# Kernel tuning notes

Measured on AMD Instinct MI355X. Metric: run time of the kernel, lower is better.

The kernel has to match this reference:

```python
import jax, jax.numpy as jnp
import numpy as np

K = 20  # hard-coded in DGCNN.__init__

def _pd_neg(x):
    # negative squared pairwise distance, [B,N,C] -> [B,N,N]
    inner = jnp.einsum('bnc,bmc->bnm', x, x)
    sq = jnp.sum(x * x, axis=-1)
    return 2.0 * inner - sq[:, :, None] - sq[:, None, :]

def _knn(x):
    return jax.lax.top_k(_pd_neg(x), K)[1]  # [B,N,K]

def _edge_feat(x, idx):
    # x: [B,N,C], idx: [B,N,K] -> [B,N,K,2C] = concat(central, neighbor-central)
    nb = jax.vmap(lambda p, i: p[i])(x, idx)
    c = x[:, :, None, :]
    return jnp.concatenate([jnp.broadcast_to(c, nb.shape), nb - c], axis=-1)

def _conv(x, w, b, act=True):
    # 1x1 Conv2d == per-point linear; BN at inference with init stats is identity
    y = jnp.einsum('...c,cd->...d', x, w) + b
    return jax.nn.relu(y) if act else y

def _forward(x, tw1, tb1, tw2, tb2, tw3, tb3, tfw1, tfb1, tfw2, tfb2, txw, txb,
             e1w1, e1b1, e1w2, e1b2, e2w1, e2b1, e2w2, e2b2, e3w1, e3b1,
             c1w, c1b, c2w, c2b, c3w, c3b, c4w, c4b):
    pts = x[:, :, :3]
    # spatial transform net on edge features of raw xyz
    ef = _edge_feat(pts, _knn(pts))                      # [B,N,K,6]
    t = _conv(_conv(ef, tw1, tb1), tw2, tb2)
    t = jnp.max(t, axis=2)                               # max over neighbors
    t = _conv(t, tw3, tb3)                               # [B,N,1024]
    t = jnp.max(t, axis=1)                               # global maxpool -> [B,1024]
    t = jax.nn.relu(t @ tfw1 + tfb1)
    t = jax.nn.relu(t @ tfw2 + tfb2)
    xf = (t @ txw + txb).reshape(-1, 3, 3)
    p = jnp.einsum('bnc,bcd->bnd', pts, xf)              # transformed points
    # EdgeConv 1
    ef = _edge_feat(p, _knn(p))                          # [B,N,K,6]
    x1 = jnp.max(_conv(_conv(ef, e1w1, e1b1), e1w2, e1b2), axis=2)   # [B,N,64]
    # EdgeConv 2
    ef = _edge_feat(x1, _knn(x1))                        # [B,N,K,128]
    x2 = jnp.max(_conv(_conv(ef, e2w1, e2b1), e2w2, e2b2), axis=2)
    # EdgeConv 3
    ef = _edge_feat(x2, _knn(x2))
    x3 = jnp.max(_conv(ef, e3w1, e3b1), axis=2)
    # global feature + per-point head
    net = _conv(jnp.concatenate([x1, x2, x3], axis=-1), c1w, c1b)    # [B,N,1024]
    g = jnp.max(net, axis=1, keepdims=True)              # maxpool over all points
    g = jnp.broadcast_to(g, (g.shape[0], x1.shape[1], g.shape[2]))
    net = jnp.concatenate([g, x1, x2, x3], axis=-1)      # [B,N,1216]
    net = _conv(net, c2w, c2b)
    net = _conv(net, c3w, c3b)
    # dropout is identity at inference (training=False)
    return _conv(net, c4w, c4b, act=False)               # [B,N,num_classes]

def setup_inputs():
    keys = iter(jax.random.split(jax.random.key(0), 64))
    def w(*shape):
        return jax.random.normal(next(keys), shape, jnp.float32) / np.float32(np.sqrt(shape[0]))
    def b(n):
        return 0.01 * jax.random.normal(next(keys), (n,), jnp.float32)
    B, N, F = 4, 4096, 6
    d = dict(x=jax.random.normal(next(keys), (B, N, F), jnp.float32))
    d.update(tw1=w(6, 64), tb1=b(64), tw2=w(64, 128), tb2=b(128), tw3=w(128, 1024), tb3=b(1024),
             tfw1=w(1024, 512), tfb1=b(512), tfw2=w(512, 256), tfb2=b(256),
             txw=0.01 * w(256, 9), txb=jnp.eye(3, dtype=jnp.float32).reshape(9))
    d.update(e1w1=w(6, 64), e1b1=b(64), e1w2=w(64, 64), e1b2=b(64),
             e2w1=w(128, 64), e2b1=b(64), e2w2=w(64, 64), e2b2=b(64),
             e3w1=w(128, 64), e3b1=b(64))
    d.update(c1w=w(192, 1024), c1b=b(1024), c2w=w(1216, 512), c2b=b(512),
             c3w=w(512, 256), c3b=b(256), c4w=w(256, 2), c4b=b(2))
    return d

def reference(x, tw1, tb1, tw2, tb2, tw3, tb3, tfw1, tfb1, tfw2, tfb2, txw, txb,
              e1w1, e1b1, e1w2, e1b2, e2w1, e2b1, e2w2, e2b2, e3w1, e3b1,
              c1w, c1b, c2w, c2b, c3w, c3b, c4w, c4b):
    return _forward(x, tw1, tb1, tw2, tb2, tw3, tb3, tfw1, tfb1, tfw2, tfb2, txw, txb,
                    e1w1, e1b1, e1w2, e1b2, e2w1, e2b1, e2w2, e2b2, e3w1, e3b1,
                    c1w, c1b, c2w, c2b, c3w, c3b, c4w, c4b)
```

## Files before the change

kernel.cpp:

```cpp
#include <hip/hip_runtime.h>

#define Nn 4096
#define KK 20
#define BN 16384

typedef __attribute__((ext_vector_type(8))) short bf16x8;
typedef __attribute__((ext_vector_type(4))) float f32x4;

__device__ __forceinline__ unsigned short f2bf(float f) {
  unsigned int x = __float_as_uint(f);
  return (unsigned short)((x + 0x7fffu + ((x >> 16) & 1u)) >> 16);
}
__device__ __forceinline__ float bf2f(unsigned short u) {
  return __uint_as_float(((unsigned int)u) << 16);
}

#define INS5(dd, tt)                                                         \
  if (dd > m5) {                                                             \
    if (dd > m3) {                                                           \
      if (dd > m1) { m5=m4;t5=t4; m4=m3;t4=t3; m3=m2;t3=t2; m2=m1;t2=t1; m1=dd;t1=tt; } \
      else if (dd > m2) { m5=m4;t5=t4; m4=m3;t4=t3; m3=m2;t3=t2; m2=dd;t2=tt; } \
      else { m5=m4;t5=t4; m4=m3;t4=t3; m3=dd;t3=tt; }                        \
    } else if (dd > m4) { m5=m4;t5=t4; m4=dd;t4=tt; }                        \
    else { m5=dd; t5=tt; }                                                   \
  }

__device__ __forceinline__ void cvtT_j(const float* __restrict__ src,
                                       unsigned short* __restrict__ dst,
                                       int N, int K, int ldn, int row0, int i) {
  if (i >= N * K) return;
  int n = i / K, k = i - n * K;
  dst[i] = f2bf(src[(size_t)(row0 + k) * ldn + n]);
}
__device__ __forceinline__ void cvtT3_j(const float* __restrict__ src,
                                        unsigned short* __restrict__ h,
                                        unsigned short* __restrict__ m,
                                        unsigned short* __restrict__ l,
                                        int N, int K, int ldn, int i) {
  if (i >= N * K) return;
  int n = i / K, k = i - n * K;
  float x = src[(size_t)k * ldn + n];
  unsigned short hh = f2bf(x); float xh = bf2f(hh);
  unsigned short mm = f2bf(x - xh); float xm = bf2f(mm);
  unsigned short ll = f2bf(x - xh - xm);
  h[i] = hh; m[i] = mm; l[i] = ll;
}
__device__ __forceinline__ void prepD_j(const float* __restrict__ w1,
                                        float* __restrict__ Md, int i) {
  if (i >= 8192) return;
  int j = i >> 7, c = i & 127;
  Md[i] = (c < 64) ? (w1[j * 64 + c] - w1[(64 + j) * 64 + c]) : w1[(64 + j) * 64 + (c - 64)];
}

__global__ __launch_bounds__(256) void k_prepAll(
    const float* __restrict__ xin, float* __restrict__ pts,
    const float* __restrict__ W22, unsigned short* __restrict__ c1wT,
    const float* __restrict__ W24, unsigned short* __restrict__ c2wT,
    const float* __restrict__ W26, unsigned short* __restrict__ c3wT,
    const float* __restrict__ W4, unsigned short* __restrict__ w3Th,
    unsigned short* __restrict__ w3Tm, unsigned short* __restrict__ w3Tl,
    const float* __restrict__ W2, unsigned short* __restrict__ tw2h,
    unsigned short* __restrict__ tw2m, unsigned short* __restrict__ tw2l,
    const float* __restrict__ W14, unsigned short* __restrict__ e1h,
    unsigned short* __restrict__ e1m, unsigned short* __restrict__ e1l,
    const float* __restrict__ W18, unsigned short* __restrict__ e2h,
    unsigned short* __restrict__ e2m, unsigned short* __restrict__ e2l,
    const float* __restrict__ W6, unsigned short* __restrict__ fw1h,
    unsigned short* __restrict__ fw1m, unsigned short* __restrict__ fw1l,
    unsigned short* __restrict__ cw2h, unsigned short* __restrict__ cw2m,
    unsigned short* __restrict__ cw2l,
    const float* __restrict__ W8, unsigned short* __restrict__ fw2h,
    unsigned short* __restrict__ fw2m, unsigned short* __restrict__ fw2l,
    const float* __restrict__ W16, float* __restrict__ MdC,
    const float* __restrict__ W20, float* __restrict__ MdD) {
  int blk = blockIdx.x, t = threadIdx.x;
  if (blk < 768) { cvtT_j(W22, c1wT, 1024, 192, 1024, 0, blk * 256 + t); return; }
  blk -= 768;
  if (blk < 384) { cvtT_j(W24, c2wT, 512, 192, 512, 1024, blk * 256 + t); return; }
  blk -= 384;
  if (blk < 512) { cvtT_j(W26, c3wT, 256, 512, 256, 0, blk * 256 + t); return; }
  blk -= 512;
  if (blk < 512) { cvtT3_j(W4, w3Th, w3Tm, w3Tl, 1024, 128, 1024, blk * 256 + t); return; }
  blk -= 512;
  if (blk < 32) { cvtT3_j(W2, tw2h, tw2m, tw2l, 128, 64, 128, blk * 256 + t); return; }
  blk -= 32;
  if (blk < 16) { cvtT3_j(W14, e1h, e1m, e1l, 64, 64, 64, blk * 256 + t); return; }
  blk -= 16;
  if (blk < 16) { cvtT3_j(W18, e2h, e2m, e2l, 64, 64, 64, blk * 256 + t); return; }
  blk -= 16;
  if (blk < 2048) { cvtT3_j(W6, fw1h, fw1m, fw1l, 512, 1024, 512, blk * 256 + t); return; }
  blk -= 2048;
  if (blk < 2048) { cvtT3_j(W24, cw2h, cw2m, cw2l, 512, 1024, 512, blk * 256 + t); return; }
  blk -= 2048;
  if (blk < 512) { cvtT3_j(W8, fw2h, fw2m, fw2l, 256, 512, 256, blk * 256 + t); return; }
  blk -= 512;
  if (blk < 32) { prepD_j(W16, MdC, blk * 256 + t); return; }
  blk -= 32;
  if (blk < 32) { prepD_j(W20, MdD, blk * 256 + t); return; }
  blk -= 32;
  {
    int i = blk * 256 + t;
    if (i < BN * 3) {
      int pt = i / 3, c = i - 3 * pt;
      pts[i] = xin[pt * 6 + c];
    }
  }
}

__global__ void k_tv3(const float* __restrict__ part, const float* __restrict__ bias,
                      unsigned short* __restrict__ h, unsigned short* __restrict__ m,
                      unsigned short* __restrict__ l) {
  int i = blockIdx.x * 256 + threadIdx.x;
  if (i >= 16 * 1024) return;
  int row = i >> 10, col = i & 1023;
  float v = 0.f;
  if (row < 4) {
    float mx = -INFINITY;
#pragma unroll 8
    for (int s = 0; s < 32; ++s) mx = fmaxf(mx, part[((size_t)row * 32 + s) * 1024 + col]);
    v = fmaxf(mx + bias[col], 0.f);
  }
  unsigned short hh = f2bf(v); float xh = bf2f(hh);
  unsigned short mm = f2bf(v - xh); float xm = bf2f(mm);
  unsigned short ll = f2bf(v - xh - xm);
  h[i] = hh; m[i] = mm; l[i] = ll;
}

__global__ void k_pad3(const float* __restrict__ src, int rows, int cols,
                       unsigned short* __restrict__ h, unsigned short* __restrict__ m,
                       unsigned short* __restrict__ l) {
  int i = blockIdx.x * 256 + threadIdx.x;
  if (i >= 16 * cols) return;
  int row = i / cols, col = i - row * cols;
  float v = (row < rows) ? src[(size_t)row * cols + col] : 0.f;
  unsigned short hh = f2bf(v); float xh = bf2f(hh);
  unsigned short mm = f2bf(v - xh); float xm = bf2f(mm);
  unsigned short ll = f2bf(v - xh - xm);
  h[i] = hh; m[i] = mm; l[i] = ll;
}

template <int N, int K, int SEG>
__global__ __launch_bounds__(256) void k_gemmSK(const unsigned short* __restrict__ Ah,
                                                const unsigned short* __restrict__ Am,
                                                const unsigned short* __restrict__ Al,
                                                const unsigned short* __restrict__ Bh,
                                                const unsigned short* __restrict__ Bm,
                                                const unsigned short* __restrict__ Bl,
                                                float* __restrict__ partial) {
  constexpr int KSEG = K / SEG;
  constexpr int KS = KSEG / 32;
  int t = threadIdx.x;
  int wv = t >> 6, lane = t & 63;
  int quad = lane >> 4, l16 = lane & 15;
  int bx = blockIdx.x;
  int nb = bx / SEG, seg = bx - nb * SEG;
  int col = nb * 64 + wv * 16 + l16;
  int k0 = seg * KSEG;
  size_t wo = (size_t)col * K + k0 + quad * 8;
  size_t ao = (size_t)l16 * K + k0 + quad * 8;
  f32x4 acc = {0.f, 0.f, 0.f, 0.f};
#pragma unroll
  for (int s = 0; s < KS; ++s) {
    bf16x8 xh = *(const bf16x8*)(Ah + ao + s * 32);
    bf16x8 xm = *(const bf16x8*)(Am + ao + s * 32);
    bf16x8 xl = *(const bf16x8*)(Al + ao + s * 32);
    bf16x8 wh = *(const bf16x8*)(Bh + wo + s * 32);
    bf16x8 wm = *(const bf16x8*)(Bm + wo + s * 32);
    bf16x8 wl = *(const bf16x8*)(Bl + wo + s * 32);
    acc = __builtin_amdgcn_mfma_f32_16x16x32_bf16(xh, wh, acc, 0, 0, 0);
    acc = __builtin_amdgcn_mfma_f32_16x16x32_bf16(xh, wm, acc, 0, 0, 0);
    acc = __builtin_amdgcn_mfma_f32_16x16x32_bf16(xm, wh, acc, 0, 0, 0);
    acc = __builtin_amdgcn_mfma_f32_16x16x32_bf16(xh, wl, acc, 0, 0, 0);
    acc = __builtin_amdgcn_mfma_f32_16x16x32_bf16(xl, wh, acc, 0, 0, 0);
    acc = __builtin_amdgcn_mfma_f32_16x16x32_bf16(xm, wm, acc, 0, 0, 0);
  }
  if (quad == 0) {
#pragma unroll
    for (int r = 0; r < 4; ++r)
      partial[((size_t)seg * 4 + r) * N + col] = acc[r];
  }
}

__global__ void k_redS(const float* __restrict__ partial, const float* __restrict__ bias,
                       float* __restrict__ outp, int N, int SEG, int relu) {
  int i = blockIdx.x * 256 + threadIdx.x;
  if (i >= 4 * N) return;
  int r = i / N, c = i - r * N;
  float s = 0.f;
  for (int seg = 0; seg < SEG; ++seg) s += partial[((size_t)seg * 4 + r) * N + c];
  if (bias) s += bias[c];
  if (relu) s = fmaxf(s, 0.f);
  outp[(size_t)r * N + c] = s;
}

__global__ __launch_bounds__(256) void k_fc3p(const float* __restrict__ h2, const float* __restrict__ txw,
                                              const float* __restrict__ txb, const float* __restrict__ pts,
                                              float* __restrict__ p) {
  __shared__ float sh2[256];
  __shared__ float sxf[9];
  int t = threadIdx.x;
  int b = blockIdx.x;
  sh2[t] = h2[(size_t)b * 256 + t];
  __syncthreads();
  if (t < 9) {
    float acc = txb[t];
    for (int j = 0; j < 256; ++j) acc = fmaf(sh2[j], txw[j * 9 + t], acc);
    sxf[t] = acc;
  }
  __syncthreads();
  for (int n = t; n < Nn; n += 256) {
    const float* pr = pts + ((size_t)b * Nn + n) * 3;
    float a0 = pr[0], a1 = pr[1], a2 = pr[2];
    float* po = p + ((size_t)b * Nn + n) * 3;
#pragma unroll
    for (int d = 0; d < 3; ++d) po[d] = a0 * sxf[d] + a1 * sxf[3 + d] + a2 * sxf[6 + d];
  }
}

__device__ __forceinline__ float dist4(const float4* __restrict__ tile4, int c,
                                       float qx, float qy, float qz, float qsq) {
  float4 v = tile4[c];
  float dot = fmaf(qx, v.x, fmaf(qy, v.y, qz * v.z));
  return 2.0f * dot - qsq - v.w;
}

__global__ __launch_bounds__(1024) void k_knn3(const float* __restrict__ src, int* __restrict__ idx) {
  __shared__ float4 tile4[Nn];
  int t = threadIdx.x;
  int wave = t >> 6, lane = t & 63;
  int g = blockIdx.x * 16 + wave;
  int b = g >> 12, n = g & (Nn - 1);
  const float* base = src + (size_t)b * Nn * 3;
  for (int e = t; e < Nn; e += 1024) {
    float x = base[e * 3], y = base[e * 3 + 1], z = base[e * 3 + 2];
    tile4[e] = make_float4(x, y, z, fmaf(x, x, fmaf(y, y, z * z)));
  }
  __syncthreads();
  float4 q4 = tile4[n];
  float qx = q4.x, qy = q4.y, qz = q4.z, qsq = q4.w;
  float m1 = -INFINITY, m2 = -INFINITY, m3 = -INFINITY, m4 = -INFINITY, m5 = -INFINITY;
  int t1 = 0, t2 = 0, t3 = 0, t4 = 0, t5 = 0;
#pragma unroll 4
  for (int tt = 0; tt < 64; ++tt) {
    float dd = dist4(tile4, (tt << 6) + lane, qx, qy, qz, qsq);
    INS5(dd, tt)
  }
  unsigned long long removed = 0ull;
  int cnt = 5;
  int sel = 0;
#pragma unroll 1
  for (int k = 0; k < 20; ++k) {
    float v = m1; int ci = (t1 << 6) | lane;
    float mx = v;
#pragma unroll
    for (int off = 32; off; off >>= 1) mx = fmaxf(mx, __shfl_xor(mx, off, 64));
    int cand = (v == mx) ? ci : 0x7FFFFFFF;
#pragma unroll
    for (int off = 32; off; off >>= 1) cand = min(cand, __shfl_xor(cand, off, 64));
    if (k == lane) sel = cand;
    if (cand == ci) {
      removed |= 1ull << t1;
      if (cnt > 1) { m1 = m2; t1 = t2; m2 = m3; t2 = t3; m3 = m4; t3 = t4; m4 = m5; t4 = t5; --cnt; }
      else {
        m1 = -INFINITY; m2 = -INFINITY; m3 = -INFINITY; m4 = -INFINITY; m5 = -INFINITY;
        t1 = 0; t2 = 0; t3 = 0; t4 = 0; t5 = 0;
#pragma unroll 1
        for (int tt = 0; tt < 64; ++tt) {
          if ((removed >> tt) & 1ull) continue;
          float dd = dist4(tile4, (tt << 6) + lane, qx, qy, qz, qsq);
          INS5(dd, tt)
        }
        cnt = 5;
      }
    }
  }
  if (lane < 20) idx[(size_t)g * KK + lane] = sel;
}

__global__ void k_sqnorm(const float* __restrict__ src, float* __restrict__ out) {
  int g = blockIdx.x * 256 + threadIdx.x;
  if (g >= BN) return;
  const float4* r = (const float4*)(src + (size_t)g * 64);
  float s = 0.f;
#pragma unroll
  for (int j = 0; j < 16; ++j) { float4 v = r[j]; s += v.x * v.x + v.y * v.y + v.z * v.z + v.w * v.w; }
  out[g] = s;
}

__device__ __forceinline__ void topk_d5(const float (&d)[64],
                                        float m1, int t1, float m2, int t2, float m3, int t3,
                                        float m4, int t4, float m5, int t5,
                                        int lane, int* __restrict__ op) {
  unsigned long long removed = 0ull;
  int cnt = 5;
  int sel = 0;
#pragma unroll 1
  for (int k = 0; k < 20; ++k) {
    float v = m1; int ci = (t1 << 6) | lane;
    float mx = v;
#pragma unroll
    for (int off = 32; off; off >>= 1) mx = fmaxf(mx, __shfl_xor(mx, off, 64));
    int cand = (v == mx) ? ci : 0x7FFFFFFF;
#pragma unroll
    for (int off = 32; off; off >>= 1) cand = min(cand, __shfl_xor(cand, off, 64));
    if (k == lane) sel = cand;
    if (cand == ci) {
      removed |= 1ull << t1;
      if (cnt > 1) { m1 = m2; t1 = t2; m2 = m3; t2 = t3; m3 = m4; t3 = t4; m4 = m5; t4 = t5; --cnt; }
      else {
        m1 = -INFINITY; m2 = -INFINITY; m3 = -INFINITY; m4 = -INFINITY; m5 = -INFINITY;
        t1 = 0; t2 = 0; t3 = 0; t4 = 0; t5 = 0;
#pragma unroll
        for (int tt = 0; tt < 64; ++tt) {
          if (!((removed >> tt) & 1ull)) {
            float dd = d[tt];
            INS5(dd, tt)
          }
        }
        cnt = 5;
      }
    }
  }
  if (lane < 20) op[lane] = sel;
}

__global__ __launch_bounds__(1024) void k_dsel(const unsigned short* __restrict__ Xh,
                                               const unsigned short* __restrict__ Xm,
                                               const unsigned short* __restrict__ Xl,
                                               const float* __restrict__ sq,
                                               int* __restrict__ idx) {
  __shared__ float sD[16 * 1284];
  int t = threadIdx.x;
  int wave = t >> 6, lane = t & 63;
  int quad = lane >> 4, l16 = lane & 15;
  int blk = blockIdx.x;
  int b = blk >> 8, rs = blk & 255;
  int r0 = rs * 16;
  const size_t base = (size_t)b * Nn * 64;
  const float* sqb = sq + b * Nn;
  bf16x8 ah[2], am[2], al[2];
#pragma unroll
  for (int ks = 0; ks < 2; ++ks) {
    size_t ra = base + (size_t)(r0 + l16) * 64 + ks * 32 + quad * 8;
    ah[ks] = *(const bf16x8*)(Xh + ra);
    am[ks] = *(const bf16x8*)(Xm + ra);
    al[ks] = *(const bf16x8*)(Xl + ra);
  }
  float sqr[4];
#pragma unroll
  for (int r = 0; r < 4; ++r) sqr[r] = sqb[r0 + quad * 4 + r];
  float d[64];
  float m1 = -INFINITY, m2 = -INFINITY, m3 = -INFINITY, m4 = -INFINITY, m5 = -INFINITY;
  int t1 = 0, t2 = 0, t3 = 0, t4 = 0, t5 = 0;
#pragma unroll
  for (int ch = 0; ch < 4; ++ch) {
#pragma unroll
    for (int tt = 0; tt < 4; ++tt) {
      int cc = wave * 64 + tt * 16;
      int cb = ch * 1024 + cc;
      f32x4 acc = {0.f, 0.f, 0.f, 0.f};
#pragma unroll
      for (int ks = 0; ks < 2; ++ks) {
        size_t rb = base + (size_t)(cb + l16) * 64 + ks * 32 + quad * 8;
        bf16x8 bh = *(const bf16x8*)(Xh + rb);
        bf16x8 bm = *(const bf16x8*)(Xm + rb);
        bf16x8 bl = *(const bf16x8*)(Xl + rb);
        acc = __builtin_amdgcn_mfma_f32_16x16x32_bf16(ah[ks], bh, acc, 0, 0, 0);
        acc = __builtin_amdgcn_mfma_f32_16x16x32_bf16(ah[ks], bm, acc, 0, 0, 0);
        acc = __builtin_amdgcn_mfma_f32_16x16x32_bf16(am[ks], bh, acc, 0, 0, 0);
        acc = __builtin_amdgcn_mfma_f32_16x16x32_bf16(ah[ks], bl, acc, 0, 0, 0);
        acc = __builtin_amdgcn_mfma_f32_16x16x32_bf16(al[ks], bh, acc, 0, 0, 0);
        acc = __builtin_amdgcn_mfma_f32_16x16x32_bf16(am[ks], bm, acc, 0, 0, 0);
      }
      float sqc = sqb[cb + l16];
#pragma unroll
      for (int r = 0; r < 4; ++r)
        sD[(quad * 4 + r) * 1284 + cc + l16] = 2.0f * acc[r] - sqr[r] - sqc;
    }
    __syncthreads();
#pragma unroll
    for (int jj = 0; jj < 16; ++jj) {
      int tt = ch * 16 + jj;
      float dd = sD[wave * 1284 + jj * 64 + lane];
      d[tt] = dd;
      INS5(dd, tt)
    }
    __syncthreads();
  }
  topk_d5(d, m1, t1, m2, t2, m3, t3, m4, t4, m5, t5, lane,
          idx + (size_t)(b * Nn + r0 + wave) * KK);
}

__global__ __launch_bounds__(256) void k_uv3(const float* __restrict__ pts, const float* __restrict__ w1,
                                             const float* __restrict__ b1, float* __restrict__ uvb) {
  __shared__ float sw[384];
  __shared__ float sb[64];
  int t = threadIdx.x;
  for (int e = t; e < 384; e += 256) sw[e] = w1[e];
  if (t < 64) sb[t] = b1[t];
  __syncthreads();
  int pl = t >> 6, c = t & 63;
  int p = blockIdx.x * 4 + pl;
  const float* pr = pts + (size_t)p * 3;
  float x0 = pr[0], x1 = pr[1], x2 = pr[2];
  float wb0 = sw[192 + c], wb1 = sw[256 + c], wb2 = sw[320 + c];
  float v = x0 * wb0 + x1 * wb1 + x2 * wb2;
  float u = sb[c] + x0 * (sw[c] - wb0) + x1 * (sw[64 + c] - wb1) + x2 * (sw[128 + c] - wb2);
  uvb[(size_t)p * 128 + c] = u;
  uvb[(size_t)p * 128 + 64 + c] = v;
}

__global__ __launch_bounds__(256) void k_uv(const float* __restrict__ x2, const float* __restrict__ Md,
                                            const float* __restrict__ bias, float* __restrict__ uv) {
  __shared__ float sM[8192];
  __shared__ float sx[32 * 68];
  int t = threadIdx.x;
  for (int e = t; e < 8192; e += 256) sM[e] = Md[e];
  int p0 = blockIdx.x * 32;
  for (int e = t; e < 512; e += 256) {
    int r = e >> 4, c4 = e & 15;
    *(float4*)(sx + r * 68 + c4 * 4) = *(const float4*)(x2 + (size_t)(p0 + r) * 64 + c4 * 4);
  }
  __syncthreads();
  int c = t & 127, rg = t >> 7;
  float badd = (c < 64) ? bias[c] : 0.f;
  float accv[16];
#pragma unroll
  for (int r = 0; r < 16; ++r) accv[r] = 0.f;
#pragma unroll
  for (int jc = 0; jc < 8; ++jc) {
    float mreg[8];
#pragma unroll
    for (int q = 0; q < 8; ++q) mreg[q] = sM[(jc * 8 + q) * 128 + c];
#pragma unroll
    for (int r = 0; r < 16; ++r) {
      const float* xr = sx + (rg * 16 + r) * 68 + jc * 8;
      float4 a = *(const float4*)xr, bb = *(const float4*)(xr + 4);
      float s = accv[r];
      s = fmaf(a.x, mreg[0], s); s = fmaf(a.y, mreg[1], s);
      s = fmaf(a.z, mreg[2], s); s = fmaf(a.w, mreg[3], s);
      s = fmaf(bb.x, mreg[4], s); s = fmaf(bb.y, mreg[5], s);
      s = fmaf(bb.z, mreg[6], s); s = fmaf(bb.w, mreg[7], s);
      accv[r] = s;
    }
  }
#pragma unroll
  for (int r = 0; r < 16; ++r)
    uv[(size_t)(p0 + rg * 16 + r) * 128 + c] = accv[r] + badd;
}

template <int NOUT, bool WRITEF, bool SPLIT3, bool CAT>
__global__ __launch_bounds__(256, 4) void k_econv(const float* __restrict__ uv,
                                                  const int* __restrict__ idx,
                                                  const unsigned short* __restrict__ W2h,
                                                  const unsigned short* __restrict__ W2m,
                                                  const unsigned short* __restrict__ W2l,
                                                  const float* __restrict__ b2,
                                                  float* __restrict__ outF,
                                                  unsigned short* __restrict__ oh,
                                                  unsigned short* __restrict__ om,
                                                  unsigned short* __restrict__ ol,
                                                  unsigned short* __restrict__ ocat,
                                                  int catoff) {
  __shared__ unsigned short y3[4][3][20 * 72];
  int t = threadIdx.x;
  int wv = t >> 6, lane = t & 63;
  int quad = lane >> 4, l16 = lane & 15;
  int p0 = blockIdx.x * 4;
  int p = p0 + wv;
  size_t nbase = (size_t)(p >> 12) * Nn;
  constexpr int CT = NOUT / 64;
  bf16x8 wfh[CT][2], wfm[CT][2], wfl[CT][2];
#pragma unroll
  for (int ct = 0; ct < CT; ++ct)
#pragma unroll
    for (int ks = 0; ks < 2; ++ks) {
      size_t wo = (size_t)(wv * (CT * 16) + ct * 16 + l16) * 64 + ks * 32 + quad * 8;
      wfh[ct][ks] = *(const bf16x8*)(W2h + wo);
      wfm[ct][ks] = *(const bf16x8*)(W2m + wo);
      wfl[ct][ks] = *(const bf16x8*)(W2l + wo);
    }
  const int* ip = idx + (size_t)p * KK;
  float u = uv[(size_t)p * 128 + lane];
  unsigned short* yh = y3[wv][0];
  unsigned short* ym = y3[wv][1];
  unsigned short* yl = y3[wv][2];
  float vv[20];
#pragma unroll
  for (int k = 0; k < 20; ++k) {
    int nb = ip[k];
    vv[k] = uv[(nbase + nb) * 128 + 64 + lane];
  }
#pragma unroll
  for (int k = 0; k < 20; ++k) {
    float y = fmaxf(u + vv[k], 0.f);
    unsigned short hh = f2bf(y); float fh = bf2f(hh);
    unsigned short mm = f2bf(y - fh); float fm = bf2f(mm);
    unsigned short ll = f2bf(y - fh - fm);
    yh[k * 72 + lane] = hh;
    ym[k * 72 + lane] = mm;
    yl[k * 72 + lane] = ll;
  }
  __syncthreads();
#pragma unroll 1
  for (int pp = 0; pp < 4; ++pp) {
    const unsigned short* ph0 = y3[pp][0];
    const unsigned short* pm0 = y3[pp][1];
    const unsigned short* pl0 = y3[pp][2];
    f32x4 acc[CT][2];
#pragma unroll
    for (int ct = 0; ct < CT; ++ct) {
      acc[ct][0] = (f32x4){0.f, 0.f, 0.f, 0.f};
      acc[ct][1] = (f32x4){0.f, 0.f, 0.f, 0.f};
    }
#pragma unroll
    for (int ks = 0; ks < 2; ++ks) {
      bf16x8 ah[2], am[2], al[2];
#pragma unroll
      for (int mt = 0; mt < 2; ++mt) {
        int row = mt * 16 + l16;
        int rr = (row < 20) ? row : 0;
        int aoff = rr * 72 + ks * 32 + quad * 8;
        ah[mt] = *(const bf16x8*)(ph0 + aoff);
        am[mt] = *(const bf16x8*)(pm0 + aoff);
        al[mt] = *(const bf16x8*)(pl0 + aoff);
      }
#pragma unroll
      for (int ct = 0; ct < CT; ++ct)
#pragma unroll
        for (int mt = 0; mt < 2; ++mt) {
          f32x4 a = acc[ct][mt];
          a = __builtin_amdgcn_mfma_f32_16x16x32_bf16(ah[mt], wfh[ct][ks], a, 0, 0, 0);
          a = __builtin_amdgcn_mfma_f32_16x16x32_bf16(ah[mt], wfm[ct][ks], a, 0, 0, 0);
          a = __builtin_amdgcn_mfma_f32_16x16x32_bf16(am[mt], wfh[ct][ks], a, 0, 0, 0);
          a = __builtin_amdgcn_mfma_f32_16x16x32_bf16(ah[mt], wfl[ct][ks], a, 0, 0, 0);
          a = __builtin_amdgcn_mfma_f32_16x16x32_bf16(al[mt], wfh[ct][ks], a, 0, 0, 0);
          a = __builtin_amdgcn_mfma_f32_16x16x32_bf16(am[mt], wfm[ct][ks], a, 0, 0, 0);
          acc[ct][mt] = a;
        }
    }
    int pt = p0 + pp;
#pragma unroll
    for (int ct = 0; ct < CT; ++ct) {
      int col = wv * (CT * 16) + ct * 16 + l16;
      float m0 = fmaxf(fmaxf(acc[ct][0][0], acc[ct][0][1]), fmaxf(acc[ct][0][2], acc[ct][0][3]));
      float m1v = (quad == 0)
                      ? fmaxf(fmaxf(acc[ct][1][0], acc[ct][1][1]), fmaxf(acc[ct][1][2], acc[ct][1][3]))
                      : -INFINITY;
      float m = fmaxf(m0, m1v);
      m = fmaxf(m, __shfl_xor(m, 16, 64));
      m = fmaxf(m, __shfl_xor(m, 32, 64));
      if (quad == 0) {
        float v = fmaxf(m + b2[col], 0.f);
        if (WRITEF) outF[(size_t)pt * NOUT + col] = v;
        if (SPLIT3) {
          unsigned short hh = f2bf(v); float fh = bf2f(hh);
          unsigned short mm2 = f2bf(v - fh); float fm = bf2f(mm2);
          unsigned short ll = f2bf(v - fh - fm);
          oh[(size_t)pt * NOUT + col] = hh;
          om[(size_t)pt * NOUT + col] = mm2;
          ol[(size_t)pt * NOUT + col] = ll;
        }
        if (CAT) ocat[(size_t)pt * 192 + catoff + col] = f2bf(v);
      }
    }
  }
}

__global__ __launch_bounds__(256) void k_gmax(const float* __restrict__ uv, const int* __restrict__ idx,
                                              unsigned short* __restrict__ ocat) {
  __shared__ int sidx[4][20];
  int t = threadIdx.x;
  int pl = t >> 6, c = t & 63;
  int p0 = blockIdx.x * 4;
  if (t < 80) sidx[t / 20][t % 20] = idx[(size_t)(p0 + t / 20) * KK + (t % 20)];
  __syncthreads();
  int p = p0 + pl;
  size_t nbase = (size_t)(p >> 12) * Nn;
  float u = uv[(size_t)p * 128 + c];
  float m = -INFINITY;
#pragma unroll
  for (int k = 0; k < 20; ++k) m = fmaxf(m, uv[(nbase + sidx[pl][k]) * 128 + 64 + c]);
  ocat[(size_t)p * 192 + 128 + c] = f2bf(fmaxf(u + m, 0.f));
}

template <int K>
__global__ __launch_bounds__(256) void k_mgemm(const unsigned short* __restrict__ A,
                                               const unsigned short* __restrict__ WT,
                                               float* __restrict__ outp) {
  constexpr int KS = K / 32;
  int t = threadIdx.x;
  int wv = t >> 6, lane = t & 63;
  int quad = lane >> 4, l16 = lane & 15;
  int blk = blockIdx.x;
  int b = blk >> 9, cb = (blk >> 5) & 15, ns = blk & 31;
  int n0 = cb * 64 + wv * 16;
  bf16x8 bfr[KS];
  const unsigned short* wrow = WT + (size_t)(n0 + l16) * K + quad * 8;
#pragma unroll
  for (int s = 0; s < KS; ++s) bfr[s] = *(const bf16x8*)(wrow + s * 32);
  const unsigned short* Ab = A + ((size_t)b * Nn + ns * 128 + l16) * K + quad * 8;
  float rmax = -INFINITY;
#pragma unroll 2
  for (int mt = 0; mt < 8; ++mt) {
    const unsigned short* ar = Ab + (size_t)mt * 16 * K;
    f32x4 acc = {0.f, 0.f, 0.f, 0.f};
#pragma unroll
    for (int s = 0; s < KS; ++s) {
      bf16x8 af = *(const bf16x8*)(ar + s * 32);
      acc = __builtin_amdgcn_mfma_f32_16x16x32_bf16(af, bfr[s], acc, 0, 0, 0);
    }
    rmax = fmaxf(rmax, fmaxf(fmaxf(acc[0], acc[1]), fmaxf(acc[2], acc[3])));
  }
  rmax = fmaxf(rmax, __shfl_xor(rmax, 16, 64));
  rmax = fmaxf(rmax, __shfl_xor(rmax, 32, 64));
  if (quad == 0) outp[((size_t)b * 32 + ns) * 1024 + n0 + l16] = rmax;
}

template <int K>
__global__ __launch_bounds__(256) void k_mgemm3s(const unsigned short* __restrict__ Ah,
                                                 const unsigned short* __restrict__ Am,
                                                 const unsigned short* __restrict__ Al,
                                                 const unsigned short* __restrict__ Bh,
                                                 const unsigned short* __restrict__ Bm,
                                                 const unsigned short* __restrict__ Bl,
                                                 float* __restrict__ outp) {
  constexpr int KS = K / 32;
  int t = threadIdx.x;
  int wv = t >> 6, lane = t & 63;
  int quad = lane >> 4, l16 = lane & 15;
  int blk = blockIdx.x;
  int b = blk >> 9, cb = (blk >> 5) & 15, ns = blk & 31;
  int n0 = cb * 64 + wv * 16;
  bf16x8 wh[KS], wm[KS], wl[KS];
  size_t wo = (size_t)(n0 + l16) * K + quad * 8;
#pragma unroll
  for (int s = 0; s < KS; ++s) {
    wh[s] = *(const bf16x8*)(Bh + wo + s * 32);
    wm[s] = *(const bf16x8*)(Bm + wo + s * 32);
    wl[s] = *(const bf16x8*)(Bl + wo + s * 32);
  }
  size_t ao = ((size_t)b * Nn + ns * 128 + l16) * K + quad * 8;
  float rmax = -INFINITY;
#pragma unroll 1
  for (int mt = 0; mt < 8; ++mt) {
    size_t ar = ao + (size_t)mt * 16 * K;
    f32x4 acc = {0.f, 0.f, 0.f, 0.f};
#pragma unroll
    for (int s = 0; s < KS; ++s) {
      bf16x8 xh = *(const bf16x8*)(Ah + ar + s * 32);
      bf16x8 xm = *(const bf16x8*)(Am + ar + s * 32);
      bf16x8 xl = *(const bf16x8*)(Al + ar + s * 32);
      acc = __builtin_amdgcn_mfma_f32_16x16x32_bf16(xh, wh[s], acc, 0, 0, 0);
      acc = __builtin_amdgcn_mfma_f32_16x16x32_bf16(xh, wm[s], acc, 0, 0, 0);
      acc = __builtin_amdgcn_mfma_f32_16x16x32_bf16(xm, wh[s], acc, 0, 0, 0);
      acc = __builtin_amdgcn_mfma_f32_16x16x32_bf16(xh, wl[s], acc, 0, 0, 0);
      acc = __builtin_amdgcn_mfma_f32_16x16x32_bf16(xl, wh[s], acc, 0, 0, 0);
      acc = __builtin_amdgcn_mfma_f32_16x16x32_bf16(xm, wm[s], acc, 0, 0, 0);
    }
    rmax = fmaxf(rmax, fmaxf(fmaxf(acc[0], acc[1]), fmaxf(acc[2], acc[3])));
  }
  rmax = fmaxf(rmax, __shfl_xor(rmax, 16, 64));
  rmax = fmaxf(rmax, __shfl_xor(rmax, 32, 64));
  if (quad == 0) outp[((size_t)b * 32 + ns) * 1024 + n0 + l16] = rmax;
}

__global__ __launch_bounds__(256) void k_final(const unsigned short* __restrict__ xcat,
                                               const float* __restrict__ gc,
                                               const float* __restrict__ c2b,
                                               const unsigned short* __restrict__ c2wT,
                                               const unsigned short* __restrict__ c3wT,
                                               const float* __restrict__ c3b,
                                               const float* __restrict__ c4w, const float* __restrict__ c4b,
                                               float* __restrict__ out) {
  __shared__ unsigned short z5[16 * 520];
  __shared__ float z2[16 * 260];
  int t = threadIdx.x;
  int wv = t >> 6, lane = t & 63;
  int quad = lane >> 4, l16 = lane & 15;
  int p0 = blockIdx.x * 16;
  int b = p0 >> 12;
  bf16x8 a1[6];
  const unsigned short* ar = xcat + (size_t)(p0 + l16) * 192 + quad * 8;
#pragma unroll
  for (int s = 0; s < 6; ++s) a1[s] = *(const bf16x8*)(ar + s * 32);
#pragma unroll 1
  for (int ntw = 0; ntw < 8; ++ntw) {
    int col = wv * 128 + ntw * 16 + l16;
    float bias = gc[(size_t)b * 512 + col] + c2b[col];
    f32x4 acc = {bias, bias, bias, bias};
    const unsigned short* wr = c2wT + (size_t)col * 192 + quad * 8;
#pragma unroll
    for (int s = 0; s < 6; ++s) {
      bf16x8 bfr = *(const bf16x8*)(wr + s * 32);
      acc = __builtin_amdgcn_mfma_f32_16x16x32_bf16(a1[s], bfr, acc, 0, 0, 0);
    }
#pragma unroll
    for (int r = 0; r < 4; ++r)
      z5[(quad * 4 + r) * 520 + col] = f2bf(fmaxf(acc[r], 0.f));
  }
  __syncthreads();
  bf16x8 a2[16];
#pragma unroll
  for (int s = 0; s < 16; ++s) a2[s] = *(const bf16x8*)(z5 + l16 * 520 + s * 32 + quad * 8);
#pragma unroll 1
  for (int ntw = 0; ntw < 4; ++ntw) {
    int col = wv * 64 + ntw * 16 + l16;
    float bias = c3b[col];
    f32x4 acc = {bias, bias, bias, bias};
    const unsigned short* wr = c3wT + (size_t)col * 512 + quad * 8;
#pragma unroll
    for (int s = 0; s < 16; ++s) {
      bf16x8 bfr = *(const bf16x8*)(wr + s * 32);
      acc = __builtin_amdgcn_mfma_f32_16x16x32_bf16(a2[s], bfr, acc, 0, 0, 0);
    }
#pragma unroll
    for (int r = 0; r < 4; ++r)
      z2[(quad * 4 + r) * 260 + col] = fmaxf(acc[r], 0.f);
  }
  __syncthreads();
  if (t < 32) {
    int m = t >> 1, e = t & 1;
    float acc = c4b[e];
    const float* zr = z2 + m * 260;
    for (int j = 0; j < 256; ++j) acc = fmaf(zr[j], c4w[j * 2 + e], acc);
    out[(size_t)(p0 + m) * 2 + e] = acc;
  }
}

extern "C" void kernel_launch(void* const* d_in, const int* in_sizes, int n_in,
                              void* d_out, int out_size, void* d_ws, size_t ws_size,
                              hipStream_t stream) {
  const float* xin = (const float*)d_in[0];
  const float* W[30];
  for (int i = 0; i < 30; ++i) W[i] = (const float*)d_in[i + 1];

  float* ws = (float*)d_ws;
  size_t off = 0;
  float* pts   = ws + off; off += (size_t)BN * 3;
  float* p     = ws + off; off += (size_t)BN * 3;
  int*   idx   = (int*)(ws + off); off += (size_t)BN * KK;
  float* sq    = ws + off; off += BN;
  float* dpart = ws + off; off += 4 * 32 * 1024;
  float* h1    = ws + off; off += 4 * 512;
  float* h2b   = ws + off; off += 4 * 256;
  float* x1    = ws + off; off += (size_t)BN * 64;
  float* x2    = ws + off; off += (size_t)BN * 64;
  float* gpart = ws + off; off += 4 * 32 * 1024;
  float* gc    = ws + off; off += 4 * 512;
  float* uvb   = ws + off; off += (size_t)BN * 128;
  float* partial = ws + off; off += 16 * 4 * 512;
  unsigned short* xcat = (unsigned short*)(ws + off); off += (size_t)BN * 96;
  unsigned short* c1wT = (unsigned short*)(ws + off); off += 98304;
  unsigned short* c2wT = (unsigned short*)(ws + off); off += 49152;
  unsigned short* c3wT = (unsigned short*)(ws + off); off += 65536;
  unsigned short* w3Th = (unsigned short*)(ws + off); off += 65536;
  unsigned short* w3Tm = (unsigned short*)(ws + off); off += 65536;
  unsigned short* w3Tl = (unsigned short*)(ws + off); off += 65536;
  unsigned short* tw2h = (unsigned short*)(ws + off); off += 4096;
  unsigned short* tw2m = (unsigned short*)(ws + off); off += 4096;
  unsigned short* tw2l = (unsigned short*)(ws + off); off += 4096;
  unsigned short* e1h  = (unsigned short*)(ws + off); off += 2048;
  unsigned short* e1m  = (unsigned short*)(ws + off); off += 2048;
  unsigned short* e1l  = (unsigned short*)(ws + off); off += 2048;
  unsigned short* e2h  = (unsigned short*)(ws + off); off += 2048;
  unsigned short* e2m  = (unsigned short*)(ws + off); off += 2048;
  unsigned short* e2l  = (unsigned short*)(ws + off); off += 2048;
  unsigned short* xsh  = (unsigned short*)(ws + off); off += 524288;
  unsigned short* xsm  = (unsigned short*)(ws + off); off += 524288;
  unsigned short* xsl  = (unsigned short*)(ws + off); off += 524288;
  float* MdC   = ws + off; off += 8192;
  float* MdD   = ws + off; off += 8192;
  unsigned short* fw1h = (unsigned short*)(ws + off); off += 262144;
  unsigned short* fw1m = (unsigned short*)(ws + off); off += 262144;
  unsigned short* fw1l = (unsigned short*)(ws + off); off += 262144;
  unsigned short* cw2h = (unsigned short*)(ws + off); off += 262144;
  unsigned short* cw2m = (unsigned short*)(ws + off); off += 262144;
  unsigned short* cw2l = (unsigned short*)(ws + off); off += 262144;
  unsigned short* fw2h = (unsigned short*)(ws + off); off += 65536;
  unsigned short* fw2m = (unsigned short*)(ws + off); off += 65536;
  unsigned short* fw2l = (unsigned short*)(ws + off); off += 65536;
  unsigned short* tvh  = (unsigned short*)(ws + off); off += 8192;
  unsigned short* tvm  = (unsigned short*)(ws + off); off += 8192;
  unsigned short* tvl  = (unsigned short*)(ws + off); off += 8192;
  unsigned short* h13h = (unsigned short*)(ws + off); off += 4096;
  unsigned short* h13m = (unsigned short*)(ws + off); off += 4096;
  unsigned short* h13l = (unsigned short*)(ws + off); off += 4096;
  float* Dbuf  = ws + off; off += (size_t)Nn * Nn;
  unsigned short* t3h = (unsigned short*)Dbuf;
  unsigned short* t3m = t3h + (size_t)BN * 128;
  unsigned short* t3l = t3m + (size_t)BN * 128;

  k_prepAll<<<dim3(7104), dim3(256), 0, stream>>>(
      xin, pts,
      W[22], c1wT, W[24], c2wT, W[26], c3wT,
      W[4], w3Th, w3Tm, w3Tl,
      W[2], tw2h, tw2m, tw2l,
      W[14], e1h, e1m, e1l,
      W[18], e2h, e2m, e2l,
      W[6], fw1h, fw1m, fw1l,
      cw2h, cw2m, cw2l,
      W[8], fw2h, fw2m, fw2l,
      W[16], MdC, W[20], MdD);

  k_knn3<<<dim3(1024), dim3(1024), 0, stream>>>(pts, idx);
  k_uv3<<<dim3(4096), dim3(256), 0, stream>>>(pts, W[0], W[1], uvb);
  k_econv<128, false, true, false><<<dim3(4096), dim3(256), 0, stream>>>(
      uvb, idx, tw2h, tw2m, tw2l, W[3], nullptr, t3h, t3m, t3l, nullptr, 0);
  k_mgemm3s<128><<<dim3(2048), dim3(256), 0, stream>>>(t3h, t3m, t3l, w3Th, w3Tm, w3Tl, dpart);
  k_tv3<<<dim3(64), dim3(256), 0, stream>>>(dpart, W[5], tvh, tvm, tvl);
  k_gemmSK<512, 1024, 16><<<dim3(128), dim3(256), 0, stream>>>(tvh, tvm, tvl, fw1h, fw1m, fw1l, partial);
  k_redS<<<dim3(8), dim3(256), 0, stream>>>(partial, W[7], h1, 512, 16, 1);
  k_pad3<<<dim3(32), dim3(256), 0, stream>>>(h1, 4, 512, h13h, h13m, h13l);
  k_gemmSK<256, 512, 8><<<dim3(32), dim3(256), 0, stream>>>(h13h, h13m, h13l, fw2h, fw2m, fw2l, partial);
  k_redS<<<dim3(4), dim3(256), 0, stream>>>(partial, W[9], h2b, 256, 8, 1);
  k_fc3p<<<dim3(4), dim3(256), 0, stream>>>(h2b, W[10], W[11], pts, p);

  k_knn3<<<dim3(1024), dim3(1024), 0, stream>>>(p, idx);
  k_uv3<<<dim3(4096), dim3(256), 0, stream>>>(p, W[12], W[13], uvb);
  k_econv<64, true, true, true><<<dim3(4096), dim3(256), 0, stream>>>(
      uvb, idx, e1h, e1m, e1l, W[15], x1, xsh, xsm, xsl, xcat, 0);
  k_sqnorm<<<dim3(64), dim3(256), 0, stream>>>(x1, sq);
  k_dsel<<<dim3(1024), dim3(1024), 0, stream>>>(xsh, xsm, xsl, sq, idx);
  k_uv<<<dim3(512), dim3(256), 0, stream>>>(x1, MdC, W[17], uvb);
  k_econv<64, true, true, true><<<dim3(4096), dim3(256), 0, stream>>>(
      uvb, idx, e2h, e2m, e2l, W[19], x2, xsh, xsm, xsl, xcat, 64);
  k_sqnorm<<<dim3(64), dim3(256), 0, stream>>>(x2, sq);
  k_dsel<<<dim3(1024), dim3(1024), 0, stream>>>(xsh, xsm, xsl, sq, idx);
  k_uv<<<dim3(512), dim3(256), 0, stream>>>(x2, MdD, W[21], uvb);
  k_gmax<<<dim3(4096), dim3(256), 0, stream>>>(uvb, idx, xcat);

  k_mgemm<192><<<dim3(2048), dim3(256), 0, stream>>>(xcat, c1wT, gpart);
  k_tv3<<<dim3(64), dim3(256), 0, stream>>>(gpart, W[23], tvh, tvm, tvl);
  k_gemmSK<512, 1024, 16><<<dim3(128), dim3(256), 0, stream>>>(tvh, tvm, tvl, cw2h, cw2m, cw2l, partial);
  k_redS<<<dim3(8), dim3(256), 0, stream>>>(partial, nullptr, gc, 512, 16, 0);
  k_final<<<dim3(1024), dim3(256), 0, stream>>>(xcat, gc, W[25], c2wT, c3wT,
                                                W[27], W[28], W[29], (float*)d_out);
}
```

Measured before the change: 1.234 ms.

## Replace block-wide kNN select with per-wave streaming top-6 plus fallback fix kernel

The 64-dim kNN selection now gives each wave 16 query rows and streams all 4096 candidates through MFMA tiles. Each lane keeps a register top-6 per row over its column slice, with no shared-memory distance matrix and no block barriers. The 20 nearest are picked by a 16-lane shuffle merge. If a lane's 6 slots run out before 20 are chosen, the row is flagged and recomputed exactly by a separate k_dfix kernel, which costs an extra launch of 2048 mostly-empty blocks and a memset, and relies on rows being flagged only rarely.

```diff
diff --git a/kernel.cpp b/kernel.cpp
--- a/kernel.cpp
+++ b/kernel.cpp
@@ -3,6 +3,7 @@
 #define Nn 4096
 #define KK 20
 #define BN 16384
+#define FCAP 2048
 
 typedef __attribute__((ext_vector_type(8))) short bf16x8;
 typedef __attribute__((ext_vector_type(4))) float f32x4;
@@ -23,6 +24,50 @@
       else { m5=m4;t5=t4; m4=m3;t4=t3; m3=dd;t3=tt; }                        \
     } else if (dd > m4) { m5=m4;t5=t4; m4=dd;t4=tt; }                        \
     else { m5=dd; t5=tt; }                                                   \
+  }
+
+#define INS6(M1,C1,M2,C2,M3,C3,M4,C4,M5,C5,M6,C6, dd, cc)                    \
+  if (dd > M6) {                                                             \
+    if (dd > M3) {                                                           \
+      if (dd > M1) { M6=M5;C6=C5; M5=M4;C5=C4; M4=M3;C4=C3; M3=M2;C3=C2; M2=M1;C2=C1; M1=dd;C1=cc; } \
+      else if (dd > M2) { M6=M5;C6=C5; M5=M4;C5=C4; M4=M3;C4=C3; M3=M2;C3=C2; M2=dd;C2=cc; } \
+      else { M6=M5;C6=C5; M5=M4;C5=C4; M4=M3;C4=C3; M3=dd;C3=cc; }           \
+    } else if (dd > M5) {                                                    \
+      if (dd > M4) { M6=M5;C6=C5; M5=M4;C5=C4; M4=dd;C4=cc; }                \
+      else { M6=M5;C6=C5; M5=dd;C5=cc; }                                     \
+    } else { M6=dd; C6=cc; }                                                 \
+  }
+
+#define POPREG(M1,C1,M2,C2,M3,C3,M4,C4,M5,C5,M6,C6, RR)                      \
+  {                                                                          \
+    int cnt = 6; int selA = 0, selB = 0; bool fail = false;                  \
+    for (int k = 0; k < 20; ++k) {                                           \
+      float v = M1; int ci = C1;                                             \
+      float mx = v;                                                          \
+      mx = fmaxf(mx, __shfl_xor(mx, 1, 64));                                 \
+      mx = fmaxf(mx, __shfl_xor(mx, 2, 64));                                 \
+      mx = fmaxf(mx, __shfl_xor(mx, 4, 64));                                 \
+      mx = fmaxf(mx, __shfl_xor(mx, 8, 64));                                 \
+      int cand = (v == mx) ? ci : 0x7FFFFFFF;                                \
+      cand = min(cand, __shfl_xor(cand, 1, 64));                             \
+      cand = min(cand, __shfl_xor(cand, 2, 64));                             \
+      cand = min(cand, __shfl_xor(cand, 4, 64));                             \
+      cand = min(cand, __shfl_xor(cand, 8, 64));                             \
+      if (l16 == k) selA = cand;                                             \
+      if (k >= 16 && l16 == (k - 16)) selB = cand;                           \
+      if (v == mx && ci == cand) {                                           \
+        if (cnt > 1) { M1=M2;C1=C2; M2=M3;C2=C3; M3=M4;C3=C4; M4=M5;C4=C5; M5=M6;C5=C6; M6=-INFINITY; --cnt; } \
+        else { M1 = -INFINITY; if (k < 19) fail = true; }                    \
+      }                                                                      \
+    }                                                                        \
+    int rowg = r0 + quad * 4 + RR;                                           \
+    idx[(size_t)rowg * KK + l16] = selA;                                     \
+    if (l16 < 4) idx[(size_t)rowg * KK + 16 + l16] = selB;                   \
+    unsigned long long fm = __ballot(fail);                                  \
+    if (l16 == 0) {                                                          \
+      unsigned grp = (unsigned)((fm >> (quad * 16)) & 0xFFFFull);            \
+      if (grp) { int pf = atomicAdd(flagc, 1); if (pf < FCAP) flagr[pf] = rowg; } \
+    }                                                                        \
   }
 
 __device__ __forceinline__ void cvtT_j(const float* __restrict__ src,
@@ -287,10 +332,130 @@
   out[g] = s;
 }
 
-__device__ __forceinline__ void topk_d5(const float (&d)[64],
-                                        float m1, int t1, float m2, int t2, float m3, int t3,
-                                        float m4, int t4, float m5, int t5,
-                                        int lane, int* __restrict__ op) {
+__global__ __launch_bounds__(256) void k_dselW(const unsigned short* __restrict__ Xh,
+                                               const unsigned short* __restrict__ Xm,
+                                               const unsigned short* __restrict__ Xl,
+                                               const float* __restrict__ sq,
+                                               int* __restrict__ flagc,
+                                               int* __restrict__ flagr,
+                                               int* __restrict__ idx) {
+  int t = threadIdx.x;
+  int wv = t >> 6, lane = t & 63;
+  int quad = lane >> 4, l16 = lane & 15;
+  int gw = blockIdx.x * 4 + wv;
+  int r0 = gw * 16;
+  int b = r0 >> 12;
+  int n0 = r0 & (Nn - 1);
+  const size_t base = (size_t)b * Nn * 64;
+  const float* sqb = sq + (size_t)b * Nn;
+  bf16x8 ah[2], am[2], al[2];
+#pragma unroll
+  for (int ks = 0; ks < 2; ++ks) {
+    size_t ra = base + (size_t)(n0 + l16) * 64 + ks * 32 + quad * 8;
+    ah[ks] = *(const bf16x8*)(Xh + ra);
+    am[ks] = *(const bf16x8*)(Xm + ra);
+    al[ks] = *(const bf16x8*)(Xl + ra);
+  }
+  float sqr0 = sqb[n0 + quad * 4 + 0];
+  float sqr1 = sqb[n0 + quad * 4 + 1];
+  float sqr2 = sqb[n0 + quad * 4 + 2];
+  float sqr3 = sqb[n0 + quad * 4 + 3];
+  float aM1=-INFINITY,aM2=-INFINITY,aM3=-INFINITY,aM4=-INFINITY,aM5=-INFINITY,aM6=-INFINITY;
+  float bM1=-INFINITY,bM2=-INFINITY,bM3=-INFINITY,bM4=-INFINITY,bM5=-INFINITY,bM6=-INFINITY;
+  float cM1=-INFINITY,cM2=-INFINITY,cM3=-INFINITY,cM4=-INFINITY,cM5=-INFINITY,cM6=-INFINITY;
+  float dM1=-INFINITY,dM2=-INFINITY,dM3=-INFINITY,dM4=-INFINITY,dM5=-INFINITY,dM6=-INFINITY;
+  int aC1=0,aC2=0,aC3=0,aC4=0,aC5=0,aC6=0;
+  int bC1=0,bC2=0,bC3=0,bC4=0,bC5=0,bC6=0;
+  int cC1=0,cC2=0,cC3=0,cC4=0,cC5=0,cC6=0;
+  int dC1=0,dC2=0,dC3=0,dC4=0,dC5=0,dC6=0;
+#pragma unroll 2
+  for (int tile = 0; tile < 256; ++tile) {
+    int cb = tile * 16;
+    f32x4 acc = {0.f, 0.f, 0.f, 0.f};
+#pragma unroll
+    for (int ks = 0; ks < 2; ++ks) {
+      size_t rb = base + (size_t)(cb + l16) * 64 + ks * 32 + quad * 8;
+      bf16x8 bh = *(const bf16x8*)(Xh + rb);
+      bf16x8 bm = *(const bf16x8*)(Xm + rb);
+      bf16x8 bl = *(const bf16x8*)(Xl + rb);
+      acc = __builtin_amdgcn_mfma_f32_16x16x32_bf16(ah[ks], bh, acc, 0, 0, 0);
+      acc = __builtin_amdgcn_mfma_f32_16x16x32_bf16(ah[ks], bm, acc, 0, 0, 0);
+      acc = __builtin_amdgcn_mfma_f32_16x16x32_bf16(am[ks], bh, acc, 0, 0, 0);
+      acc = __builtin_amdgcn_mfma_f32_16x16x32_bf16(ah[ks], bl, acc, 0, 0, 0);
+      acc = __builtin_amdgcn_mfma_f32_16x16x32_bf16(al[ks], bh, acc, 0, 0, 0);
+      acc = __builtin_amdgcn_mfma_f32_16x16x32_bf16(am[ks], bm, acc, 0, 0, 0);
+    }
+    float sqc = sqb[cb + l16];
+    int cc = cb + l16;
+    float dd0 = 2.0f * acc[0] - sqr0 - sqc;
+    float dd1 = 2.0f * acc[1] - sqr1 - sqc;
+    float dd2 = 2.0f * acc[2] - sqr2 - sqc;
+    float dd3 = 2.0f * acc[3] - sqr3 - sqc;
+    INS6(aM1,aC1,aM2,aC2,aM3,aC3,aM4,aC4,aM5,aC5,aM6,aC6, dd0, cc)
+    INS6(bM1,bC1,bM2,bC2,bM3,bC3,bM4,bC4,bM5,bC5,bM6,bC6, dd1, cc)
+    INS6(cM1,cC1,cM2,cC2,cM3,cC3,cM4,cC4,cM5,cC5,cM6,cC6, dd2, cc)
+    INS6(dM1,dC1,dM2,dC2,dM3,dC3,dM4,dC4,dM5,dC5,dM6,dC6, dd3, cc)
+  }
+  POPREG(aM1,aC1,aM2,aC2,aM3,aC3,aM4,aC4,aM5,aC5,aM6,aC6, 0)
+  POPREG(bM1,bC1,bM2,bC2,bM3,bC3,bM4,bC4,bM5,bC5,bM6,bC6, 1)
+  POPREG(cM1,cC1,cM2,cC2,cM3,cC3,cM4,cC4,cM5,cC5,cM6,cC6, 2)
+  POPREG(dM1,dC1,dM2,dC2,dM3,dC3,dM4,dC4,dM5,dC5,dM6,dC6, 3)
+}
+
+__global__ __launch_bounds__(1024) void k_dfix(const unsigned short* __restrict__ Xh,
+                                               const unsigned short* __restrict__ Xm,
+                                               const unsigned short* __restrict__ Xl,
+                                               const float* __restrict__ sq,
+                                               const int* __restrict__ flagc,
+                                               const int* __restrict__ flagr,
+                                               int* __restrict__ idx) {
+  __shared__ float sRow[Nn];
+  int nf = flagc[0]; if (nf > FCAP) nf = FCAP;
+  if ((int)blockIdx.x >= nf) return;
+  int row = flagr[blockIdx.x];
+  int b = row >> 12, r = row & (Nn - 1);
+  int t = threadIdx.x;
+  int wave = t >> 6, lane = t & 63;
+  int quad = lane >> 4, l16 = lane & 15;
+  const size_t base = (size_t)b * Nn * 64;
+  const float* sqb = sq + (size_t)b * Nn;
+  bf16x8 ah[2], am[2], al[2];
+#pragma unroll
+  for (int ks = 0; ks < 2; ++ks) {
+    size_t ra = base + (size_t)r * 64 + ks * 32 + quad * 8;
+    ah[ks] = *(const bf16x8*)(Xh + ra);
+    am[ks] = *(const bf16x8*)(Xm + ra);
+    al[ks] = *(const bf16x8*)(Xl + ra);
+  }
+  float sqr = sqb[r];
+#pragma unroll 1
+  for (int tt = 0; tt < 16; ++tt) {
+    int cb = wave * 256 + tt * 16;
+    f32x4 acc = {0.f, 0.f, 0.f, 0.f};
+#pragma unroll
+    for (int ks = 0; ks < 2; ++ks) {
+      size_t rb = base + (size_t)(cb + l16) * 64 + ks * 32 + quad * 8;
+      bf16x8 bh = *(const bf16x8*)(Xh + rb);
+      bf16x8 bm = *(const bf16x8*)(Xm + rb);
+      bf16x8 bl = *(const bf16x8*)(Xl + rb);
+      acc = __builtin_amdgcn_mfma_f32_16x16x32_bf16(ah[ks], bh, acc, 0, 0, 0);
+      acc = __builtin_amdgcn_mfma_f32_16x16x32_bf16(ah[ks], bm, acc, 0, 0, 0);
+      acc = __builtin_amdgcn_mfma_f32_16x16x32_bf16(am[ks], bh, acc, 0, 0, 0);
+      acc = __builtin_amdgcn_mfma_f32_16x16x32_bf16(ah[ks], bl, acc, 0, 0, 0);
+      acc = __builtin_amdgcn_mfma_f32_16x16x32_bf16(al[ks], bh, acc, 0, 0, 0);
+      acc = __builtin_amdgcn_mfma_f32_16x16x32_bf16(am[ks], bm, acc, 0, 0, 0);
+    }
+    if (quad == 0) sRow[cb + l16] = 2.0f * acc[0] - sqr - sqb[cb + l16];
+  }
+  __syncthreads();
+  if (wave != 0) return;
+  float m1 = -INFINITY, m2 = -INFINITY, m3 = -INFINITY, m4 = -INFINITY, m5 = -INFINITY;
+  int t1 = 0, t2 = 0, t3 = 0, t4 = 0, t5 = 0;
+#pragma unroll 1
+  for (int tt = 0; tt < 64; ++tt) {
+    float dd = sRow[(tt << 6) | lane];
+    INS5(dd, tt)
+  }
   unsigned long long removed = 0ull;
   int cnt = 5;
   int sel = 0;
@@ -310,85 +475,17 @@
       else {
         m1 = -INFINITY; m2 = -INFINITY; m3 = -INFINITY; m4 = -INFINITY; m5 = -INFINITY;
         t1 = 0; t2 = 0; t3 = 0; t4 = 0; t5 = 0;
-#pragma unroll
+#pragma unroll 1
         for (int tt = 0; tt < 64; ++tt) {
-          if (!((removed >> tt) & 1ull)) {
-            float dd = d[tt];
-            INS5(dd, tt)
-          }
+          if ((removed >> tt) & 1ull) continue;
+          float dd = sRow[(tt << 6) | lane];
+          INS5(dd, tt)
         }
         cnt = 5;
       }
     }
   }
-  if (lane < 20) op[lane] = sel;
-}
-
-__global__ __launch_bounds__(1024) void k_dsel(const unsigned short* __restrict__ Xh,
-                                               const unsigned short* __restrict__ Xm,
-                                               const unsigned short* __restrict__ Xl,
-                                               const float* __restrict__ sq,
-                                               int* __restrict__ idx) {
-  __shared__ float sD[16 * 1284];
-  int t = threadIdx.x;
-  int wave = t >> 6, lane = t & 63;
-  int quad = lane >> 4, l16 = lane & 15;
-  int blk = blockIdx.x;
-  int b = blk >> 8, rs = blk & 255;
-  int r0 = rs * 16;
-  const size_t base = (size_t)b * Nn * 64;
-  const float* sqb = sq + b * Nn;
-  bf16x8 ah[2], am[2], al[2];
-#pragma unroll
-  for (int ks = 0; ks < 2; ++ks) {
-    size_t ra = base + (size_t)(r0 + l16) * 64 + ks * 32 + quad * 8;
-    ah[ks] = *(const bf16x8*)(Xh + ra);
-    am[ks] = *(const bf16x8*)(Xm + ra);
-    al[ks] = *(const bf16x8*)(Xl + ra);
-  }
-  float sqr[4];
-#pragma unroll
-  for (int r = 0; r < 4; ++r) sqr[r] = sqb[r0 + quad * 4 + r];
-  float d[64];
-  float m1 = -INFINITY, m2 = -INFINITY, m3 = -INFINITY, m4 = -INFINITY, m5 = -INFINITY;
-  int t1 = 0, t2 = 0, t3 = 0, t4 = 0, t5 = 0;
-#pragma unroll
-  for (int ch = 0; ch < 4; ++ch) {
-#pragma unroll
-    for (int tt = 0; tt < 4; ++tt) {
-      int cc = wave * 64 + tt * 16;
-      int cb = ch * 1024 + cc;
-      f32x4 acc = {0.f, 0.f, 0.f, 0.f};
-#pragma unroll
-      for (int ks = 0; ks < 2; ++ks) {
-        size_t rb = base + (size_t)(cb + l16) * 64 + ks * 32 + quad * 8;
-        bf16x8 bh = *(const bf16x8*)(Xh + rb);
-        bf16x8 bm = *(const bf16x8*)(Xm + rb);
-        bf16x8 bl = *(const bf16x8*)(Xl + rb);
-        acc = __builtin_amdgcn_mfma_f32_16x16x32_bf16(ah[ks], bh, acc, 0, 0, 0);
-        acc = __builtin_amdgcn_mfma_f32_16x16x32_bf16(ah[ks], bm, acc, 0, 0, 0);
-        acc = __builtin_amdgcn_mfma_f32_16x16x32_bf16(am[ks], bh, acc, 0, 0, 0);
-        acc = __builtin_amdgcn_mfma_f32_16x16x32_bf16(ah[ks], bl, acc, 0, 0, 0);
-        acc = __builtin_amdgcn_mfma_f32_16x16x32_bf16(al[ks], bh, acc, 0, 0, 0);
-        acc = __builtin_amdgcn_mfma_f32_16x16x32_bf16(am[ks], bm, acc, 0, 0, 0);
-      }
-      float sqc = sqb[cb + l16];
-#pragma unroll
-      for (int r = 0; r < 4; ++r)
-        sD[(quad * 4 + r) * 1284 + cc + l16] = 2.0f * acc[r] - sqr[r] - sqc;
-    }
-    __syncthreads();
-#pragma unroll
-    for (int jj = 0; jj < 16; ++jj) {
-      int tt = ch * 16 + jj;
-      float dd = sD[wave * 1284 + jj * 64 + lane];
-      d[tt] = dd;
-      INS5(dd, tt)
-    }
-    __syncthreads();
-  }
-  topk_d5(d, m1, t1, m2, t2, m3, t3, m4, t4, m5, t5, lane,
-          idx + (size_t)(b * Nn + r0 + wave) * KK);
+  if (lane < 20) idx[(size_t)row * KK + lane] = sel;
 }
 
 __global__ __launch_bounds__(256) void k_uv3(const float* __restrict__ pts, const float* __restrict__ w1,
@@ -750,6 +847,8 @@
   float* gc    = ws + off; off += 4 * 512;
   float* uvb   = ws + off; off += (size_t)BN * 128;
   float* partial = ws + off; off += 16 * 4 * 512;
+  int*   flagc = (int*)(ws + off); off += 16;
+  int*   flagr = (int*)(ws + off); off += FCAP;
   unsigned short* xcat = (unsigned short*)(ws + off); off += (size_t)BN * 96;
   unsigned short* c1wT = (unsigned short*)(ws + off); off += 98304;
   unsigned short* c2wT = (unsigned short*)(ws + off); off += 49152;
@@ -821,12 +920,16 @@
   k_econv<64, true, true, true><<<dim3(4096), dim3(256), 0, stream>>>(
       uvb, idx, e1h, e1m, e1l, W[15], x1, xsh, xsm, xsl, xcat, 0);
   k_sqnorm<<<dim3(64), dim3(256), 0, stream>>>(x1, sq);
-  k_dsel<<<dim3(1024), dim3(1024), 0, stream>>>(xsh, xsm, xsl, sq, idx);
+  hipMemsetAsync(flagc, 0, sizeof(int), stream);
+  k_dselW<<<dim3(256), dim3(256), 0, stream>>>(xsh, xsm, xsl, sq, flagc, flagr, idx);
+  k_dfix<<<dim3(FCAP), dim3(1024), 0, stream>>>(xsh, xsm, xsl, sq, flagc, flagr, idx);
   k_uv<<<dim3(512), dim3(256), 0, stream>>>(x1, MdC, W[17], uvb);
   k_econv<64, true, true, true><<<dim3(4096), dim3(256), 0, stream>>>(
       uvb, idx, e2h, e2m, e2l, W[19], x2, xsh, xsm, xsl, xcat, 64);
   k_sqnorm<<<dim3(64), dim3(256), 0, stream>>>(x2, sq);
-  k_dsel<<<dim3(1024), dim3(1024), 0, stream>>>(xsh, xsm, xsl, sq, idx);
+  hipMemsetAsync(flagc, 0, sizeof(int), stream);
+  k_dselW<<<dim3(256), dim3(256), 0, stream>>>(xsh, xsm, xsl, sq, flagc, flagr, idx);
+  k_dfix<<<dim3(FCAP), dim3(1024), 0, stream>>>(xsh, xsm, xsl, sq, flagc, flagr, idx);
   k_uv<<<dim3(512), dim3(256), 0, stream>>>(x2, MdD, W[21], uvb);
   k_gmax<<<dim3(4096), dim3(256), 0, stream>>>(uvb, idx, xcat);
 
```

Measured after the change: 1.465 ms. +18.8%, slower.
